# Kernel tuning notes

Hardware: AMD Instinct MI355X
Metric: run time of the kernel (lower is better)

Reference implementation:

```python
import jax, jax.numpy as jnp
import numpy as np

B, TQ, TK, D, H = 4, 2048, 2048, 512, 8  # hidden=512, num_heads=8, head_dim=64


def setup_inputs() -> dict:
    key = jax.random.key(0)
    ks = jax.random.split(key, 7)
    s = 0.03  # small init scale for linear weights
    return {
        "q": jax.random.normal(ks[0], (B, TQ, D), jnp.float32),
        "k": jax.random.normal(ks[1], (B, TK, D), jnp.float32),
        "v": jax.random.normal(ks[2], (B, TK, D), jnp.float32),
        "Wq": jax.random.normal(ks[3], (D, D), jnp.float32) * s,
        "bq": jnp.zeros((D,), jnp.float32),
        "Wk": jax.random.normal(ks[4], (D, D), jnp.float32) * s,
        "bk": jnp.zeros((D,), jnp.float32),
        "Wv": jax.random.normal(ks[5], (D, D), jnp.float32) * s,
        "bv": jnp.zeros((D,), jnp.float32),
        "Wo": jax.random.normal(ks[6], (D, D), jnp.float32) * s,
        "bo": jnp.zeros((D,), jnp.float32),
    }


def reference(q, k, v, Wq, bq, Wk, bk, Wv, bv, Wo, bo):
    Bq, Tq, _ = q.shape
    Tk = k.shape[1]
    Dh = D // H  # head dim = 64
    # torch Linear: x @ W.T + b; split heads -> [B, H, T, Dh]
    qh = (q @ Wq.T + bq).reshape(Bq, Tq, H, Dh).transpose(0, 2, 1, 3)
    kh = (k @ Wk.T + bk).reshape(Bq, Tk, H, Dh).transpose(0, 2, 1, 3)
    vh = (v @ Wv.T + bv).reshape(Bq, Tk, H, Dh).transpose(0, 2, 1, 3)
    scale = 1.0 / float(np.sqrt(Dh))
    scores = jnp.einsum("bhqd,bhkd->bhqk", qh, kh) * scale  # [B,H,Tq,Tk]
    # causal mask: tril(ones, diagonal=Tk-Tq); log-additive masking == -inf off-band
    causal = jnp.tril(jnp.ones((Tq, Tk), bool), k=Tk - Tq)
    scores = jnp.where(causal, scores, -jnp.inf)
    w = jax.nn.softmax(scores, axis=-1)  # attention weights
    x = jnp.einsum("bhqk,bhkd->bhqd", w, vh)
    x = x.transpose(0, 2, 1, 3).reshape(Bq, Tq, D)
    return x @ Wo.T + bo, w
```

## Files before the change

kernel.cpp:

```cpp
#include <hip/hip_runtime.h>


typedef __attribute__((ext_vector_type(4))) float f32x4;
typedef __attribute__((ext_vector_type(8))) short short8;
typedef __attribute__((ext_vector_type(8))) __bf16 bf16x8;
typedef __attribute__((ext_vector_type(2))) unsigned int uintx2;
typedef __attribute__((ext_vector_type(4))) unsigned int uintx4;

static __device__ __forceinline__ unsigned short bfc(float f) {
  return __builtin_bit_cast(unsigned short, (__bf16)f);
}
static __device__ __forceinline__ unsigned pkbf(float a, float b) {
  return (unsigned)bfc(a) | ((unsigned)bfc(b) << 16);
}
static __device__ __forceinline__ short8 cvt_bf8(f32x4 f0, f32x4 f1) {
  uintx4 u;
  u[0] = pkbf(f0[0], f0[1]);
  u[1] = pkbf(f0[2], f0[3]);
  u[2] = pkbf(f1[0], f1[1]);
  u[3] = pkbf(f1[2], f1[3]);
  return __builtin_bit_cast(short8, u);
}

static __device__ __forceinline__ f32x4 mfma16(short8 a, short8 b, f32x4 c) {
  return __builtin_amdgcn_mfma_f32_16x16x32_bf16(
      __builtin_bit_cast(bf16x8, a), __builtin_bit_cast(bf16x8, b), c, 0, 0, 0);
}

#define GLD16(gsrc, ldst)                                                     \
  __builtin_amdgcn_global_load_lds(                                           \
      (const __attribute__((address_space(1))) void*)(gsrc),                  \
      (__attribute__((address_space(3))) void*)(ldst), 16, 0, 0)

template <int IN_BF16>
__device__ __forceinline__ void gemm_core(const void* __restrict__ Xv,
                                          const float* __restrict__ W,
                                          short (*As)[72], short (*Bs)[72],
                                          int row0, int col0, f32x4 (&acc)[4][4]) {
  const int tid = threadIdx.x;
  const int lane = tid & 63;
  const int wv = tid >> 6, wm = wv >> 1, wn = wv & 1;
  const int g = lane >> 4, c = lane & 15;

  for (int k0 = 0; k0 < 512; k0 += 64) {
    for (int ch = tid; ch < 1024; ch += 256) {
      const int r = ch >> 3, kc = (ch & 7) * 8;
      if (IN_BF16) {
        *(short8*)&As[r][kc] =
            *(const short8*)((const short*)Xv + (size_t)(row0 + r) * 512 + k0 + kc);
      } else {
        const float* src = (const float*)Xv + (size_t)(row0 + r) * 512 + k0 + kc;
        *(short8*)&As[r][kc] = cvt_bf8(*(const f32x4*)src, *(const f32x4*)(src + 4));
      }
      {
        const float* src = W + (size_t)(col0 + r) * 512 + k0 + kc;
        *(short8*)&Bs[r][kc] = cvt_bf8(*(const f32x4*)src, *(const f32x4*)(src + 4));
      }
    }
    __syncthreads();
#pragma unroll
    for (int kk = 0; kk < 2; ++kk) {
      short8 a[4], b[4];
#pragma unroll
      for (int i = 0; i < 4; ++i) a[i] = *(const short8*)&As[wm * 64 + i * 16 + c][kk * 32 + g * 8];
#pragma unroll
      for (int i = 0; i < 4; ++i) b[i] = *(const short8*)&Bs[wn * 64 + i * 16 + c][kk * 32 + g * 8];
#pragma unroll
      for (int mi = 0; mi < 4; ++mi)
#pragma unroll
        for (int ni = 0; ni < 4; ++ni) acc[mi][ni] = mfma16(a[mi], b[ni], acc[mi][ni]);
    }
    __syncthreads();
  }
}

__global__ __launch_bounds__(256) void qkv_gemm(
    const float* __restrict__ q, const float* __restrict__ k, const float* __restrict__ v,
    const float* __restrict__ Wq, const float* __restrict__ bq,
    const float* __restrict__ Wk, const float* __restrict__ bk,
    const float* __restrict__ Wv, const float* __restrict__ bv,
    unsigned short* __restrict__ Qbf, unsigned short* __restrict__ Kbf,
    unsigned short* __restrict__ Vbf) {
  __shared__ short As[128][72];
  __shared__ short Bs[128][72];
  const int z = blockIdx.z;
  const float* X = z == 0 ? q : (z == 1 ? k : v);
  const float* W = z == 0 ? Wq : (z == 1 ? Wk : Wv);
  const float* bias = z == 0 ? bq : (z == 1 ? bk : bv);
  const int row0 = blockIdx.x * 128, col0 = blockIdx.y * 128;

  f32x4 acc[4][4] = {};
  gemm_core<0>(X, W, As, Bs, row0, col0, acc);

  const int lane = threadIdx.x & 63;
  const int wv = threadIdx.x >> 6, wm = wv >> 1, wn = wv & 1;
  const int g = lane >> 4, c = lane & 15;

  if (z < 2) {
    unsigned short* Y = z == 0 ? Qbf : Kbf;
    const float scl = z == 0 ? 0.18033688f : 1.0f;
#pragma unroll
    for (int mi = 0; mi < 4; ++mi)
#pragma unroll
      for (int ni = 0; ni < 4; ++ni) {
        const int col = col0 + wn * 64 + ni * 16 + c;
        const float bvl = bias[col];
        const int rowb = row0 + wm * 64 + mi * 16 + g * 4;
#pragma unroll
        for (int r = 0; r < 4; ++r) {
          const int row = rowb + r;
          const int bb = row >> 11, t = row & 2047;
          const int h = col >> 6, dh = col & 63;
          Y[((size_t)((bb * 8 + h) * 2048 + t) << 6) + dh] = bfc((acc[mi][ni][r] + bvl) * scl);
        }
      }
  } else {
#pragma unroll
    for (int mi = 0; mi < 4; ++mi)
#pragma unroll
      for (int ni = 0; ni < 4; ++ni) {
        const int col = col0 + wn * 64 + ni * 16 + c;
        const float bvl = bias[col];
        const int rowb = row0 + wm * 64 + mi * 16 + g * 4;
        const int bb = rowb >> 11, t = rowb & 2047;
        const int h = col >> 6, dh = col & 63;
        uintx2 pk;
        pk[0] = pkbf(acc[mi][ni][0] + bvl, acc[mi][ni][1] + bvl);
        pk[1] = pkbf(acc[mi][ni][2] + bvl, acc[mi][ni][3] + bvl);
        *(uintx2*)(Vbf + ((size_t)((bb * 8 + h) * 64 + dh) * 2048 + t)) = pk;
      }
  }
}

__global__ __launch_bounds__(256) void out_gemm(const unsigned short* __restrict__ ctx,
                                                const float* __restrict__ Wo,
                                                const float* __restrict__ bo,
                                                float* __restrict__ out) {
  __shared__ short As[128][72];
  __shared__ short Bs[128][72];
  const int row0 = blockIdx.x * 128, col0 = blockIdx.y * 128;
  f32x4 acc[4][4] = {};
  gemm_core<1>(ctx, Wo, As, Bs, row0, col0, acc);

  const int lane = threadIdx.x & 63;
  const int wv = threadIdx.x >> 6, wm = wv >> 1, wn = wv & 1;
  const int g = lane >> 4, c = lane & 15;
#pragma unroll
  for (int mi = 0; mi < 4; ++mi)
#pragma unroll
    for (int ni = 0; ni < 4; ++ni) {
      const int col = col0 + wn * 64 + ni * 16 + c;
      const float bvl = bo[col];
      const int rowb = row0 + wm * 64 + mi * 16 + g * 4;
#pragma unroll
      for (int r = 0; r < 4; ++r) out[(size_t)(rowb + r) * 512 + col] = acc[mi][ni][r] + bvl;
    }
}

__global__ __launch_bounds__(256) void attn_kernel(
    const unsigned short* __restrict__ Qb, const unsigned short* __restrict__ Kb,
    const unsigned short* __restrict__ Vtg, unsigned short* __restrict__ ctx,
    float* __restrict__ wout) {
  __shared__ short Kd[2][8192];
  __shared__ short Vd[2][8192];
  __shared__ short Ps[4][16][128];

  const int tid = threadIdx.x, lane = tid & 63, wv = tid >> 6;
  const int g = lane >> 4, c = lane & 15;
  const int sw = (c & 7) << 3;
  const int p = blockIdx.x, bh = blockIdx.y;
  const unsigned short* Qp = Qb + (size_t)bh * (2048 * 64);
  const unsigned short* Kp = Kb + (size_t)bh * (2048 * 64);
  const unsigned short* Vp = Vtg + (size_t)bh * (64 * 2048);
  const int b_ = bh >> 3, h_ = bh & 7;

  for (int half = 0; half < 2; ++half) {
    const int t = half ? (31 - p) : p;
    const int q0 = t * 64;
    const int jmax = t >> 1;
    const int qr = q0 + wv * 16 + c;

    __syncthreads();
#pragma unroll
    for (int i = 0; i < 4; ++i) {
      const int gr = (wv * 4 + i) * 64 + lane;
      const int row = gr >> 3, slot = gr & 7;
      GLD16(Kp + ((size_t)row * 64) + ((slot ^ (row & 7)) << 3),
            (char*)Kd[0] + ((wv * 4 + i) << 10));
    }
#pragma unroll
    for (int i = 0; i < 4; ++i) {
      const int gr = (wv * 4 + i) * 64 + lane;
      const int row = gr >> 4, slot = gr & 15;
      GLD16(Vp + ((size_t)row * 2048) + ((slot ^ (row & 7)) << 3),
            (char*)Vd[0] + ((wv * 4 + i) << 10));
    }

    short8 qf[2];
    qf[0] = *(const short8*)(Qp + (size_t)qr * 64 + g * 8);
    qf[1] = *(const short8*)(Qp + (size_t)qr * 64 + 32 + g * 8);

    f32x4 O[4] = {};
    float l_r = 0.0f;

    for (int j = 0; j <= jmax; ++j) {
      __syncthreads();
      if (j < jmax) {
        const int nb = (j + 1) & 1;
#pragma unroll
        for (int i = 0; i < 4; ++i) {
          const int gr = (wv * 4 + i) * 64 + lane;
          const int row = gr >> 3, slot = gr & 7;
          GLD16(Kp + ((size_t)((j + 1) * 128 + row) * 64) + ((slot ^ (row & 7)) << 3),
                (char*)Kd[nb] + ((wv * 4 + i) << 10));
        }
#pragma unroll
        for (int i = 0; i < 4; ++i) {
          const int gr = (wv * 4 + i) * 64 + lane;
          const int row = gr >> 4, slot = gr & 15;
          GLD16(Vp + ((size_t)row * 2048) + (j + 1) * 128 + ((slot ^ (row & 7)) << 3),
                (char*)Vd[nb] + ((wv * 4 + i) << 10));
        }
      }
      const short* Ksb = Kd[j & 1];
      const short* Vsb = Vd[j & 1];

      f32x4 S[8];
#pragma unroll
      for (int nc = 0; nc < 8; ++nc) S[nc] = (f32x4){0.f, 0.f, 0.f, 0.f};
#pragma unroll
      for (int kk = 0; kk < 2; ++kk)
#pragma unroll
        for (int nc = 0; nc < 8; ++nc) {
          const int row = nc * 16 + c;
          const short8 kf = *(const short8*)&Ksb[row * 64 + (((kk * 4 + g) ^ (c & 7)) << 3)];
          S[nc] = mfma16(kf, qf[kk], S[nc]);
        }

      f32x4 ssum = {0.f, 0.f, 0.f, 0.f};
      if (j == jmax) {
        const int kvb = j * 128 + g * 4;
#pragma unroll
        for (int nc = 0; nc < 8; ++nc) {
#pragma unroll
          for (int r = 0; r < 4; ++r) {
            float val = __builtin_amdgcn_exp2f(S[nc][r]);
            if (kvb + nc * 16 + r > qr) val = 0.f;
            S[nc][r] = val;
          }
          ssum += S[nc];
        }
      } else {
#pragma unroll
        for (int nc = 0; nc < 8; ++nc) {
#pragma unroll
          for (int r = 0; r < 4; ++r) S[nc][r] = __builtin_amdgcn_exp2f(S[nc][r]);
          ssum += S[nc];
        }
      }
      l_r += ssum[0] + ssum[1] + ssum[2] + ssum[3];

#pragma unroll
      for (int nc = 0; nc < 8; ++nc) {
        uintx2 pk;
        pk[0] = pkbf(S[nc][0], S[nc][1]);
        pk[1] = pkbf(S[nc][2], S[nc][3]);
        *(uintx2*)&Ps[wv][c][(nc * 16 + g * 4) ^ sw] = pk;
      }

#pragma unroll
      for (int kk2 = 0; kk2 < 4; ++kk2) {
        const short8 pa = *(const short8*)&Ps[wv][c][(kk2 * 32 + g * 8) ^ sw];
#pragma unroll
        for (int nd = 0; nd < 4; ++nd) {
          const int row = nd * 16 + c;
          const short8 vb = *(const short8*)&Vsb[row * 128 + (((kk2 * 4 + g) ^ (c & 7)) << 3)];
          O[nd] = mfma16(pa, vb, O[nd]);
        }
      }
    }

    l_r += __shfl_xor(l_r, 16);
    l_r += __shfl_xor(l_r, 32);

    {
      float lv[4];
#pragma unroll
      for (int r = 0; r < 4; ++r) lv[r] = __shfl(l_r, g * 4 + r);
#pragma unroll
      for (int r = 0; r < 4; ++r) {
        const float inv = 1.0f / lv[r];
        const int trow = q0 + wv * 16 + g * 4 + r;
        unsigned short* cp = ctx + ((size_t)(b_ * 2048 + trow) * 512) + h_ * 64;
#pragma unroll
        for (int nd = 0; nd < 4; ++nd) cp[nd * 16 + c] = bfc(O[nd][r] * inv);
      }
    }

    const float inv_l = 1.0f / l_r;
    float* wbase = wout + ((size_t)bh * 2048 + q0) * 2048;
    for (int j = jmax; j >= 0; --j) {
      __syncthreads();
      if (j > 0) {
#pragma unroll
        for (int i = 0; i < 4; ++i) {
          const int gr = (wv * 4 + i) * 64 + lane;
          const int row = gr >> 3, slot = gr & 7;
          GLD16(Kp + ((size_t)((j - 1) * 128 + row) * 64) + ((slot ^ (row & 7)) << 3),
                (char*)Kd[(j - 1) & 1] + ((wv * 4 + i) << 10));
        }
      }
      const short* Ksb = Kd[j & 1];

      f32x4 S[8];
#pragma unroll
      for (int nc = 0; nc < 8; ++nc) S[nc] = (f32x4){0.f, 0.f, 0.f, 0.f};
#pragma unroll
      for (int kk = 0; kk < 2; ++kk)
#pragma unroll
        for (int nc = 0; nc < 8; ++nc) {
          const int row = nc * 16 + c;
          const short8 kf = *(const short8*)&Ksb[row * 64 + (((kk * 4 + g) ^ (c & 7)) << 3)];
          S[nc] = mfma16(kf, qf[kk], S[nc]);
        }

      const bool lastj = (j == jmax);
      float* wr = wbase + (size_t)(wv * 16 + c) * 2048 + j * 128;
#pragma unroll
      for (int nc = 0; nc < 8; ++nc) {
        f32x4 w4;
#pragma unroll
        for (int r = 0; r < 4; ++r) {
          float val = __builtin_amdgcn_exp2f(S[nc][r]) * inv_l;
          if (lastj && (j * 128 + nc * 16 + g * 4 + r > qr)) val = 0.f;
          w4[r] = val;
        }
        *(f32x4*)(wr + nc * 16 + g * 4) = w4;
      }
    }

    {
      const int c0 = (jmax + 1) * 128;
      const f32x4 z = {0.f, 0.f, 0.f, 0.f};
      for (int rr = wv; rr < 64; rr += 4) {
        float* rp = wbase + (size_t)rr * 2048;
        for (int x = c0 + lane * 4; x < 2048; x += 256) *(f32x4*)(rp + x) = z;
      }
    }
  }
}

extern "C" void kernel_launch(void* const* d_in, const int* in_sizes, int n_in,
                              void* d_out, int out_size, void* d_ws, size_t ws_size,
                              hipStream_t stream) {
  const float* q  = (const float*)d_in[0];
  const float* k  = (const float*)d_in[1];
  const float* v  = (const float*)d_in[2];
  const float* Wq = (const float*)d_in[3];
  const float* bq = (const float*)d_in[4];
  const float* Wk = (const float*)d_in[5];
  const float* bk = (const float*)d_in[6];
  const float* Wv = (const float*)d_in[7];
  const float* bv = (const float*)d_in[8];
  const float* Wo = (const float*)d_in[9];
  const float* bo = (const float*)d_in[10];

  unsigned short* Qbf = (unsigned short*)d_ws;
  unsigned short* Kbf = Qbf + (size_t)4194304;
  unsigned short* Vbf = Kbf + (size_t)4194304;
  unsigned short* ctx = Vbf + (size_t)4194304;

  float* out  = (float*)d_out;
  float* wout = out + (size_t)4 * 2048 * 512;

  qkv_gemm<<<dim3(64, 4, 3), 256, 0, stream>>>(q, k, v, Wq, bq, Wk, bk, Wv, bv, Qbf, Kbf, Vbf);
  attn_kernel<<<dim3(16, 32), 256, 0, stream>>>(Qbf, Kbf, Vbf, ctx, wout);
  out_gemm<<<dim3(64, 4), 256, 0, stream>>>(ctx, Wo, bo, out);
}
```

Measured before the change: 240.1 us.

## Fuse long tile's weight-output pass with short tile's forward pass sharing K loads

The attention kernel handles a long and a short query tile per block. It now fuses the long tile's second pass (recompute scores, write normalized weights) into the short tile's forward pass, so each K tile staged into LDS feeds both query tiles. The aim is to cut the number of K tile loads and barrier-separated iterations per block. In exchange it keeps both Q fragment sets live and doubles the score accumulators in the fused loop, which raises register pressure.

```diff
diff --git a/kernel.cpp b/kernel.cpp
--- a/kernel.cpp
+++ b/kernel.cpp
@@ -157,6 +157,27 @@
     }
 }
 
+static __device__ __forceinline__ void stage_k(const unsigned short* __restrict__ Kp,
+                                               short* dst, int j, int wv, int lane) {
+#pragma unroll
+  for (int i = 0; i < 4; ++i) {
+    const int gr = (wv * 4 + i) * 64 + lane;
+    const int row = gr >> 3, slot = gr & 7;
+    GLD16(Kp + ((size_t)(j * 128 + row) * 64) + ((slot ^ (row & 7)) << 3),
+          (char*)dst + ((wv * 4 + i) << 10));
+  }
+}
+static __device__ __forceinline__ void stage_v(const unsigned short* __restrict__ Vp,
+                                               short* dst, int j, int wv, int lane) {
+#pragma unroll
+  for (int i = 0; i < 4; ++i) {
+    const int gr = (wv * 4 + i) * 64 + lane;
+    const int row = gr >> 4, slot = gr & 15;
+    GLD16(Vp + ((size_t)row * 2048) + j * 128 + ((slot ^ (row & 7)) << 3),
+          (char*)dst + ((wv * 4 + i) << 10));
+  }
+}
+
 __global__ __launch_bounds__(256) void attn_kernel(
     const unsigned short* __restrict__ Qb, const unsigned short* __restrict__ Kb,
     const unsigned short* __restrict__ Vtg, unsigned short* __restrict__ ctx,
@@ -174,78 +195,159 @@
   const unsigned short* Vp = Vtg + (size_t)bh * (64 * 2048);
   const int b_ = bh >> 3, h_ = bh & 7;
 
-  for (int half = 0; half < 2; ++half) {
-    const int t = half ? (31 - p) : p;
-    const int q0 = t * 64;
-    const int jmax = t >> 1;
-    const int qr = q0 + wv * 16 + c;
-
+  const int tL = 31 - p, tS = p;
+  const int jL = tL >> 1, jS = tS >> 1;
+  const int q0L = tL * 64, q0S = tS * 64;
+  const int qrL = q0L + wv * 16 + c, qrS = q0S + wv * 16 + c;
+
+  short8 qfL[2], qfS[2];
+  qfL[0] = *(const short8*)(Qp + (size_t)qrL * 64 + g * 8);
+  qfL[1] = *(const short8*)(Qp + (size_t)qrL * 64 + 32 + g * 8);
+  qfS[0] = *(const short8*)(Qp + (size_t)qrS * 64 + g * 8);
+  qfS[1] = *(const short8*)(Qp + (size_t)qrS * 64 + 32 + g * 8);
+
+  float* const wbaseL = wout + ((size_t)bh * 2048 + q0L) * 2048;
+  float* const wbaseS = wout + ((size_t)bh * 2048 + q0S) * 2048;
+
+  stage_k(Kp, Kd[0], 0, wv, lane);
+  stage_v(Vp, Vd[0], 0, wv, lane);
+
+  f32x4 OL[4] = {};
+  float lL = 0.0f;
+  for (int j = 0; j <= jL; ++j) {
     __syncthreads();
-#pragma unroll
-    for (int i = 0; i < 4; ++i) {
-      const int gr = (wv * 4 + i) * 64 + lane;
-      const int row = gr >> 3, slot = gr & 7;
-      GLD16(Kp + ((size_t)row * 64) + ((slot ^ (row & 7)) << 3),
-            (char*)Kd[0] + ((wv * 4 + i) << 10));
-    }
-#pragma unroll
-    for (int i = 0; i < 4; ++i) {
-      const int gr = (wv * 4 + i) * 64 + lane;
-      const int row = gr >> 4, slot = gr & 15;
-      GLD16(Vp + ((size_t)row * 2048) + ((slot ^ (row & 7)) << 3),
-            (char*)Vd[0] + ((wv * 4 + i) << 10));
-    }
-
-    short8 qf[2];
-    qf[0] = *(const short8*)(Qp + (size_t)qr * 64 + g * 8);
-    qf[1] = *(const short8*)(Qp + (size_t)qr * 64 + 32 + g * 8);
-
-    f32x4 O[4] = {};
-    float l_r = 0.0f;
-
-    for (int j = 0; j <= jmax; ++j) {
-      __syncthreads();
-      if (j < jmax) {
-        const int nb = (j + 1) & 1;
-#pragma unroll
-        for (int i = 0; i < 4; ++i) {
-          const int gr = (wv * 4 + i) * 64 + lane;
-          const int row = gr >> 3, slot = gr & 7;
-          GLD16(Kp + ((size_t)((j + 1) * 128 + row) * 64) + ((slot ^ (row & 7)) << 3),
-                (char*)Kd[nb] + ((wv * 4 + i) << 10));
-        }
-#pragma unroll
-        for (int i = 0; i < 4; ++i) {
-          const int gr = (wv * 4 + i) * 64 + lane;
-          const int row = gr >> 4, slot = gr & 15;
-          GLD16(Vp + ((size_t)row * 2048) + (j + 1) * 128 + ((slot ^ (row & 7)) << 3),
-                (char*)Vd[nb] + ((wv * 4 + i) << 10));
-        }
-      }
-      const short* Ksb = Kd[j & 1];
+    if (j < jL) {
+      const int nb = (j + 1) & 1;
+      stage_k(Kp, Kd[nb], j + 1, wv, lane);
+      stage_v(Vp, Vd[nb], j + 1, wv, lane);
+    }
+    const short* Ksb = Kd[j & 1];
+    const short* Vsb = Vd[j & 1];
+
+    f32x4 S[8];
+#pragma unroll
+    for (int nc = 0; nc < 8; ++nc) S[nc] = (f32x4){0.f, 0.f, 0.f, 0.f};
+#pragma unroll
+    for (int kk = 0; kk < 2; ++kk)
+#pragma unroll
+      for (int nc = 0; nc < 8; ++nc) {
+        const int row = nc * 16 + c;
+        const short8 kf = *(const short8*)&Ksb[row * 64 + (((kk * 4 + g) ^ (c & 7)) << 3)];
+        S[nc] = mfma16(kf, qfL[kk], S[nc]);
+      }
+
+    f32x4 ssum = {0.f, 0.f, 0.f, 0.f};
+    if (j == jL) {
+      const int kvb = j * 128 + g * 4;
+#pragma unroll
+      for (int nc = 0; nc < 8; ++nc) {
+#pragma unroll
+        for (int r = 0; r < 4; ++r) {
+          float val = __builtin_amdgcn_exp2f(S[nc][r]);
+          if (kvb + nc * 16 + r > qrL) val = 0.f;
+          S[nc][r] = val;
+        }
+        ssum += S[nc];
+      }
+    } else {
+#pragma unroll
+      for (int nc = 0; nc < 8; ++nc) {
+#pragma unroll
+        for (int r = 0; r < 4; ++r) S[nc][r] = __builtin_amdgcn_exp2f(S[nc][r]);
+        ssum += S[nc];
+      }
+    }
+    lL += ssum[0] + ssum[1] + ssum[2] + ssum[3];
+
+#pragma unroll
+    for (int nc = 0; nc < 8; ++nc) {
+      uintx2 pk;
+      pk[0] = pkbf(S[nc][0], S[nc][1]);
+      pk[1] = pkbf(S[nc][2], S[nc][3]);
+      *(uintx2*)&Ps[wv][c][(nc * 16 + g * 4) ^ sw] = pk;
+    }
+#pragma unroll
+    for (int kk2 = 0; kk2 < 4; ++kk2) {
+      const short8 pa = *(const short8*)&Ps[wv][c][(kk2 * 32 + g * 8) ^ sw];
+#pragma unroll
+      for (int nd = 0; nd < 4; ++nd) {
+        const int row = nd * 16 + c;
+        const short8 vb = *(const short8*)&Vsb[row * 128 + (((kk2 * 4 + g) ^ (c & 7)) << 3)];
+        OL[nd] = mfma16(pa, vb, OL[nd]);
+      }
+    }
+  }
+
+  lL += __shfl_xor(lL, 16);
+  lL += __shfl_xor(lL, 32);
+  {
+    float lv[4];
+#pragma unroll
+    for (int r = 0; r < 4; ++r) lv[r] = __shfl(lL, g * 4 + r);
+#pragma unroll
+    for (int r = 0; r < 4; ++r) {
+      const float inv = 1.0f / lv[r];
+      const int trow = q0L + wv * 16 + g * 4 + r;
+      unsigned short* cp = ctx + ((size_t)(b_ * 2048 + trow) * 512) + h_ * 64;
+#pragma unroll
+      for (int nd = 0; nd < 4; ++nd) cp[nd * 16 + c] = bfc(OL[nd][r] * inv);
+    }
+  }
+  const float inv_lL = 1.0f / lL;
+
+  __syncthreads();
+  stage_k(Kp, Kd[0], 0, wv, lane);
+  stage_v(Vp, Vd[0], 0, wv, lane);
+
+  f32x4 OS[4] = {};
+  float lS = 0.0f;
+  for (int j = 0; j <= jL; ++j) {
+    __syncthreads();
+    if (j < jL) {
+      const int nb = (j + 1) & 1;
+      stage_k(Kp, Kd[nb], j + 1, wv, lane);
+      if (j + 1 <= jS) stage_v(Vp, Vd[nb], j + 1, wv, lane);
+    }
+    const short* Ksb = Kd[j & 1];
+
+    if (j <= jS) {
       const short* Vsb = Vd[j & 1];
-
-      f32x4 S[8];
-#pragma unroll
-      for (int nc = 0; nc < 8; ++nc) S[nc] = (f32x4){0.f, 0.f, 0.f, 0.f};
+      f32x4 S[8], S2[8];
+#pragma unroll
+      for (int nc = 0; nc < 8; ++nc) {
+        S[nc] = (f32x4){0.f, 0.f, 0.f, 0.f};
+        S2[nc] = (f32x4){0.f, 0.f, 0.f, 0.f};
+      }
 #pragma unroll
       for (int kk = 0; kk < 2; ++kk)
 #pragma unroll
         for (int nc = 0; nc < 8; ++nc) {
           const int row = nc * 16 + c;
           const short8 kf = *(const short8*)&Ksb[row * 64 + (((kk * 4 + g) ^ (c & 7)) << 3)];
-          S[nc] = mfma16(kf, qf[kk], S[nc]);
-        }
+          S[nc] = mfma16(kf, qfS[kk], S[nc]);
+          S2[nc] = mfma16(kf, qfL[kk], S2[nc]);
+        }
+
+      {
+        float* wr = wbaseL + (size_t)(wv * 16 + c) * 2048 + j * 128;
+#pragma unroll
+        for (int nc = 0; nc < 8; ++nc) {
+          f32x4 w4;
+#pragma unroll
+          for (int r = 0; r < 4; ++r) w4[r] = __builtin_amdgcn_exp2f(S2[nc][r]) * inv_lL;
+          *(f32x4*)(wr + nc * 16 + g * 4) = w4;
+        }
+      }
 
       f32x4 ssum = {0.f, 0.f, 0.f, 0.f};
-      if (j == jmax) {
+      if (j == jS) {
         const int kvb = j * 128 + g * 4;
 #pragma unroll
         for (int nc = 0; nc < 8; ++nc) {
 #pragma unroll
           for (int r = 0; r < 4; ++r) {
             float val = __builtin_amdgcn_exp2f(S[nc][r]);
-            if (kvb + nc * 16 + r > qr) val = 0.f;
+            if (kvb + nc * 16 + r > qrS) val = 0.f;
             S[nc][r] = val;
           }
           ssum += S[nc];
@@ -258,7 +360,7 @@
           ssum += S[nc];
         }
       }
-      l_r += ssum[0] + ssum[1] + ssum[2] + ssum[3];
+      lS += ssum[0] + ssum[1] + ssum[2] + ssum[3];
 
 #pragma unroll
       for (int nc = 0; nc < 8; ++nc) {
@@ -267,7 +369,6 @@
         pk[1] = pkbf(S[nc][2], S[nc][3]);
         *(uintx2*)&Ps[wv][c][(nc * 16 + g * 4) ^ sw] = pk;
       }
-
 #pragma unroll
       for (int kk2 = 0; kk2 < 4; ++kk2) {
         const short8 pa = *(const short8*)&Ps[wv][c][(kk2 * 32 + g * 8) ^ sw];
@@ -275,77 +376,98 @@
         for (int nd = 0; nd < 4; ++nd) {
           const int row = nd * 16 + c;
           const short8 vb = *(const short8*)&Vsb[row * 128 + (((kk2 * 4 + g) ^ (c & 7)) << 3)];
-          O[nd] = mfma16(pa, vb, O[nd]);
-        }
-      }
-    }
-
-    l_r += __shfl_xor(l_r, 16);
-    l_r += __shfl_xor(l_r, 32);
-
-    {
-      float lv[4];
-#pragma unroll
-      for (int r = 0; r < 4; ++r) lv[r] = __shfl(l_r, g * 4 + r);
-#pragma unroll
-      for (int r = 0; r < 4; ++r) {
-        const float inv = 1.0f / lv[r];
-        const int trow = q0 + wv * 16 + g * 4 + r;
-        unsigned short* cp = ctx + ((size_t)(b_ * 2048 + trow) * 512) + h_ * 64;
-#pragma unroll
-        for (int nd = 0; nd < 4; ++nd) cp[nd * 16 + c] = bfc(O[nd][r] * inv);
-      }
-    }
-
-    const float inv_l = 1.0f / l_r;
-    float* wbase = wout + ((size_t)bh * 2048 + q0) * 2048;
-    for (int j = jmax; j >= 0; --j) {
-      __syncthreads();
-      if (j > 0) {
-#pragma unroll
-        for (int i = 0; i < 4; ++i) {
-          const int gr = (wv * 4 + i) * 64 + lane;
-          const int row = gr >> 3, slot = gr & 7;
-          GLD16(Kp + ((size_t)((j - 1) * 128 + row) * 64) + ((slot ^ (row & 7)) << 3),
-                (char*)Kd[(j - 1) & 1] + ((wv * 4 + i) << 10));
-        }
-      }
-      const short* Ksb = Kd[j & 1];
-
-      f32x4 S[8];
-#pragma unroll
-      for (int nc = 0; nc < 8; ++nc) S[nc] = (f32x4){0.f, 0.f, 0.f, 0.f};
+          OS[nd] = mfma16(pa, vb, OS[nd]);
+        }
+      }
+    } else {
+      f32x4 S2[8];
+#pragma unroll
+      for (int nc = 0; nc < 8; ++nc) S2[nc] = (f32x4){0.f, 0.f, 0.f, 0.f};
 #pragma unroll
       for (int kk = 0; kk < 2; ++kk)
 #pragma unroll
         for (int nc = 0; nc < 8; ++nc) {
           const int row = nc * 16 + c;
           const short8 kf = *(const short8*)&Ksb[row * 64 + (((kk * 4 + g) ^ (c & 7)) << 3)];
-          S[nc] = mfma16(kf, qf[kk], S[nc]);
-        }
-
-      const bool lastj = (j == jmax);
-      float* wr = wbase + (size_t)(wv * 16 + c) * 2048 + j * 128;
+          S2[nc] = mfma16(kf, qfL[kk], S2[nc]);
+        }
+      const bool lastj = (j == jL);
+      float* wr = wbaseL + (size_t)(wv * 16 + c) * 2048 + j * 128;
 #pragma unroll
       for (int nc = 0; nc < 8; ++nc) {
         f32x4 w4;
 #pragma unroll
         for (int r = 0; r < 4; ++r) {
-          float val = __builtin_amdgcn_exp2f(S[nc][r]) * inv_l;
-          if (lastj && (j * 128 + nc * 16 + g * 4 + r > qr)) val = 0.f;
+          float val = __builtin_amdgcn_exp2f(S2[nc][r]) * inv_lL;
+          if (lastj && (j * 128 + nc * 16 + g * 4 + r > qrL)) val = 0.f;
           w4[r] = val;
         }
         *(f32x4*)(wr + nc * 16 + g * 4) = w4;
       }
     }
-
-    {
-      const int c0 = (jmax + 1) * 128;
-      const f32x4 z = {0.f, 0.f, 0.f, 0.f};
-      for (int rr = wv; rr < 64; rr += 4) {
-        float* rp = wbase + (size_t)rr * 2048;
-        for (int x = c0 + lane * 4; x < 2048; x += 256) *(f32x4*)(rp + x) = z;
-      }
+  }
+
+  lS += __shfl_xor(lS, 16);
+  lS += __shfl_xor(lS, 32);
+  {
+    float lv[4];
+#pragma unroll
+    for (int r = 0; r < 4; ++r) lv[r] = __shfl(lS, g * 4 + r);
+#pragma unroll
+    for (int r = 0; r < 4; ++r) {
+      const float inv = 1.0f / lv[r];
+      const int trow = q0S + wv * 16 + g * 4 + r;
+      unsigned short* cp = ctx + ((size_t)(b_ * 2048 + trow) * 512) + h_ * 64;
+#pragma unroll
+      for (int nd = 0; nd < 4; ++nd) cp[nd * 16 + c] = bfc(OS[nd][r] * inv);
+    }
+  }
+  const float inv_lS = 1.0f / lS;
+
+  __syncthreads();
+  stage_k(Kp, Kd[0], 0, wv, lane);
+  for (int j = 0; j <= jS; ++j) {
+    __syncthreads();
+    if (j < jS) stage_k(Kp, Kd[(j + 1) & 1], j + 1, wv, lane);
+    const short* Ksb = Kd[j & 1];
+
+    f32x4 S2[8];
+#pragma unroll
+    for (int nc = 0; nc < 8; ++nc) S2[nc] = (f32x4){0.f, 0.f, 0.f, 0.f};
+#pragma unroll
+    for (int kk = 0; kk < 2; ++kk)
+#pragma unroll
+      for (int nc = 0; nc < 8; ++nc) {
+        const int row = nc * 16 + c;
+        const short8 kf = *(const short8*)&Ksb[row * 64 + (((kk * 4 + g) ^ (c & 7)) << 3)];
+        S2[nc] = mfma16(kf, qfS[kk], S2[nc]);
+      }
+    const bool lastj = (j == jS);
+    float* wr = wbaseS + (size_t)(wv * 16 + c) * 2048 + j * 128;
+#pragma unroll
+    for (int nc = 0; nc < 8; ++nc) {
+      f32x4 w4;
+#pragma unroll
+      for (int r = 0; r < 4; ++r) {
+        float val = __builtin_amdgcn_exp2f(S2[nc][r]) * inv_lS;
+        if (lastj && (j * 128 + nc * 16 + g * 4 + r > qrS)) val = 0.f;
+        w4[r] = val;
+      }
+      *(f32x4*)(wr + nc * 16 + g * 4) = w4;
+    }
+  }
+
+  {
+    const f32x4 z = {0.f, 0.f, 0.f, 0.f};
+    const int c0L = (jL + 1) * 128;
+    for (int rr = wv; rr < 64; rr += 4) {
+      float* rp = wbaseL + (size_t)rr * 2048;
+      for (int x = c0L + lane * 4; x < 2048; x += 256) *(f32x4*)(rp + x) = z;
+    }
+    const int c0S = (jS + 1) * 128;
+    for (int rr = wv; rr < 64; rr += 4) {
+      float* rp = wbaseS + (size_t)rr * 2048;
+      for (int x = c0S + lane * 4; x < 2048; x += 256) *(f32x4*)(rp + x) = z;
     }
   }
 }
```

Result: slower. 268.5 us (+11.9%).

## Shrink attention KV tile to 64 columns, raise occupancy, use nontemporal weight stores

Applied to the files above, without the earlier changes.

The attention kernel's key/value tile shrinks from 128 to 64 columns, which halves the LDS buffers, and launch bounds now request 4 blocks per SM for more occupancy. The causal diagonal block now matches the 64-row query tile, so less masked work is computed on the last block. The attention-weight and zero-fill stores become nontemporal to avoid polluting the cache. The cost is twice as many loop iterations and barriers, plus possible register pressure from the occupancy bound.

```diff
diff --git a/kernel.cpp b/kernel.cpp
--- a/kernel.cpp
+++ b/kernel.cpp
@@ -157,13 +157,34 @@
     }
 }
 
-__global__ __launch_bounds__(256) void attn_kernel(
+static __device__ __forceinline__ void stage_k64(const unsigned short* __restrict__ Kp,
+                                                 short* dst, int j, int wv, int lane) {
+#pragma unroll
+  for (int i = 0; i < 2; ++i) {
+    const int gr = (wv * 2 + i) * 64 + lane;
+    const int row = gr >> 3, slot = gr & 7;
+    GLD16(Kp + ((size_t)(j * 64 + row) * 64) + ((slot ^ (row & 7)) << 3),
+          (char*)dst + ((wv * 2 + i) << 10));
+  }
+}
+static __device__ __forceinline__ void stage_v64(const unsigned short* __restrict__ Vp,
+                                                 short* dst, int j, int wv, int lane) {
+#pragma unroll
+  for (int i = 0; i < 2; ++i) {
+    const int gr = (wv * 2 + i) * 64 + lane;
+    const int row = gr >> 3, slot = gr & 7;
+    GLD16(Vp + ((size_t)row * 2048) + j * 64 + ((slot ^ (row & 7)) << 3),
+          (char*)dst + ((wv * 2 + i) << 10));
+  }
+}
+
+__global__ __launch_bounds__(256, 4) void attn_kernel(
     const unsigned short* __restrict__ Qb, const unsigned short* __restrict__ Kb,
     const unsigned short* __restrict__ Vtg, unsigned short* __restrict__ ctx,
     float* __restrict__ wout) {
-  __shared__ short Kd[2][8192];
-  __shared__ short Vd[2][8192];
-  __shared__ short Ps[4][16][128];
+  __shared__ short Kd[2][4096];
+  __shared__ short Vd[2][4096];
+  __shared__ short Ps[4][16][64];
 
   const int tid = threadIdx.x, lane = tid & 63, wv = tid >> 6;
   const int g = lane >> 4, c = lane & 15;
@@ -177,24 +198,12 @@
   for (int half = 0; half < 2; ++half) {
     const int t = half ? (31 - p) : p;
     const int q0 = t * 64;
-    const int jmax = t >> 1;
+    const int jmax = t;
     const int qr = q0 + wv * 16 + c;
 
     __syncthreads();
-#pragma unroll
-    for (int i = 0; i < 4; ++i) {
-      const int gr = (wv * 4 + i) * 64 + lane;
-      const int row = gr >> 3, slot = gr & 7;
-      GLD16(Kp + ((size_t)row * 64) + ((slot ^ (row & 7)) << 3),
-            (char*)Kd[0] + ((wv * 4 + i) << 10));
-    }
-#pragma unroll
-    for (int i = 0; i < 4; ++i) {
-      const int gr = (wv * 4 + i) * 64 + lane;
-      const int row = gr >> 4, slot = gr & 15;
-      GLD16(Vp + ((size_t)row * 2048) + ((slot ^ (row & 7)) << 3),
-            (char*)Vd[0] + ((wv * 4 + i) << 10));
-    }
+    stage_k64(Kp, Kd[0], 0, wv, lane);
+    stage_v64(Vp, Vd[0], 0, wv, lane);
 
     short8 qf[2];
     qf[0] = *(const short8*)(Qp + (size_t)qr * 64 + g * 8);
@@ -207,31 +216,19 @@
       __syncthreads();
       if (j < jmax) {
         const int nb = (j + 1) & 1;
-#pragma unroll
-        for (int i = 0; i < 4; ++i) {
-          const int gr = (wv * 4 + i) * 64 + lane;
-          const int row = gr >> 3, slot = gr & 7;
-          GLD16(Kp + ((size_t)((j + 1) * 128 + row) * 64) + ((slot ^ (row & 7)) << 3),
-                (char*)Kd[nb] + ((wv * 4 + i) << 10));
-        }
-#pragma unroll
-        for (int i = 0; i < 4; ++i) {
-          const int gr = (wv * 4 + i) * 64 + lane;
-          const int row = gr >> 4, slot = gr & 15;
-          GLD16(Vp + ((size_t)row * 2048) + (j + 1) * 128 + ((slot ^ (row & 7)) << 3),
-                (char*)Vd[nb] + ((wv * 4 + i) << 10));
-        }
+        stage_k64(Kp, Kd[nb], j + 1, wv, lane);
+        stage_v64(Vp, Vd[nb], j + 1, wv, lane);
       }
       const short* Ksb = Kd[j & 1];
       const short* Vsb = Vd[j & 1];
 
-      f32x4 S[8];
-#pragma unroll
-      for (int nc = 0; nc < 8; ++nc) S[nc] = (f32x4){0.f, 0.f, 0.f, 0.f};
+      f32x4 S[4];
+#pragma unroll
+      for (int nc = 0; nc < 4; ++nc) S[nc] = (f32x4){0.f, 0.f, 0.f, 0.f};
 #pragma unroll
       for (int kk = 0; kk < 2; ++kk)
 #pragma unroll
-        for (int nc = 0; nc < 8; ++nc) {
+        for (int nc = 0; nc < 4; ++nc) {
           const int row = nc * 16 + c;
           const short8 kf = *(const short8*)&Ksb[row * 64 + (((kk * 4 + g) ^ (c & 7)) << 3)];
           S[nc] = mfma16(kf, qf[kk], S[nc]);
@@ -239,9 +236,9 @@
 
       f32x4 ssum = {0.f, 0.f, 0.f, 0.f};
       if (j == jmax) {
-        const int kvb = j * 128 + g * 4;
-#pragma unroll
-        for (int nc = 0; nc < 8; ++nc) {
+        const int kvb = j * 64 + g * 4;
+#pragma unroll
+        for (int nc = 0; nc < 4; ++nc) {
 #pragma unroll
           for (int r = 0; r < 4; ++r) {
             float val = __builtin_amdgcn_exp2f(S[nc][r]);
@@ -252,7 +249,7 @@
         }
       } else {
 #pragma unroll
-        for (int nc = 0; nc < 8; ++nc) {
+        for (int nc = 0; nc < 4; ++nc) {
 #pragma unroll
           for (int r = 0; r < 4; ++r) S[nc][r] = __builtin_amdgcn_exp2f(S[nc][r]);
           ssum += S[nc];
@@ -261,7 +258,7 @@
       l_r += ssum[0] + ssum[1] + ssum[2] + ssum[3];
 
 #pragma unroll
-      for (int nc = 0; nc < 8; ++nc) {
+      for (int nc = 0; nc < 4; ++nc) {
         uintx2 pk;
         pk[0] = pkbf(S[nc][0], S[nc][1]);
         pk[1] = pkbf(S[nc][2], S[nc][3]);
@@ -269,12 +266,12 @@
       }
 
 #pragma unroll
-      for (int kk2 = 0; kk2 < 4; ++kk2) {
+      for (int kk2 = 0; kk2 < 2; ++kk2) {
         const short8 pa = *(const short8*)&Ps[wv][c][(kk2 * 32 + g * 8) ^ sw];
 #pragma unroll
         for (int nd = 0; nd < 4; ++nd) {
           const int row = nd * 16 + c;
-          const short8 vb = *(const short8*)&Vsb[row * 128 + (((kk2 * 4 + g) ^ (c & 7)) << 3)];
+          const short8 vb = *(const short8*)&Vsb[row * 64 + (((kk2 * 4 + g) ^ (c & 7)) << 3)];
           O[nd] = mfma16(pa, vb, O[nd]);
         }
       }
@@ -301,50 +298,43 @@
     float* wbase = wout + ((size_t)bh * 2048 + q0) * 2048;
     for (int j = jmax; j >= 0; --j) {
       __syncthreads();
-      if (j > 0) {
-#pragma unroll
-        for (int i = 0; i < 4; ++i) {
-          const int gr = (wv * 4 + i) * 64 + lane;
-          const int row = gr >> 3, slot = gr & 7;
-          GLD16(Kp + ((size_t)((j - 1) * 128 + row) * 64) + ((slot ^ (row & 7)) << 3),
-                (char*)Kd[(j - 1) & 1] + ((wv * 4 + i) << 10));
-        }
-      }
+      if (j > 0) stage_k64(Kp, Kd[(j - 1) & 1], j - 1, wv, lane);
       const short* Ksb = Kd[j & 1];
 
-      f32x4 S[8];
-#pragma unroll
-      for (int nc = 0; nc < 8; ++nc) S[nc] = (f32x4){0.f, 0.f, 0.f, 0.f};
+      f32x4 S[4];
+#pragma unroll
+      for (int nc = 0; nc < 4; ++nc) S[nc] = (f32x4){0.f, 0.f, 0.f, 0.f};
 #pragma unroll
       for (int kk = 0; kk < 2; ++kk)
 #pragma unroll
-        for (int nc = 0; nc < 8; ++nc) {
+        for (int nc = 0; nc < 4; ++nc) {
           const int row = nc * 16 + c;
           const short8 kf = *(const short8*)&Ksb[row * 64 + (((kk * 4 + g) ^ (c & 7)) << 3)];
           S[nc] = mfma16(kf, qf[kk], S[nc]);
         }
 
       const bool lastj = (j == jmax);
-      float* wr = wbase + (size_t)(wv * 16 + c) * 2048 + j * 128;
-#pragma unroll
-      for (int nc = 0; nc < 8; ++nc) {
+      float* wr = wbase + (size_t)(wv * 16 + c) * 2048 + j * 64;
+#pragma unroll
+      for (int nc = 0; nc < 4; ++nc) {
         f32x4 w4;
 #pragma unroll
         for (int r = 0; r < 4; ++r) {
           float val = __builtin_amdgcn_exp2f(S[nc][r]) * inv_l;
-          if (lastj && (j * 128 + nc * 16 + g * 4 + r > qr)) val = 0.f;
+          if (lastj && (j * 64 + nc * 16 + g * 4 + r > qr)) val = 0.f;
           w4[r] = val;
         }
-        *(f32x4*)(wr + nc * 16 + g * 4) = w4;
+        __builtin_nontemporal_store(w4, (f32x4*)(wr + nc * 16 + g * 4));
       }
     }
 
     {
-      const int c0 = (jmax + 1) * 128;
+      const int c0 = (jmax + 1) * 64;
       const f32x4 z = {0.f, 0.f, 0.f, 0.f};
       for (int rr = wv; rr < 64; rr += 4) {
         float* rp = wbase + (size_t)rr * 2048;
-        for (int x = c0 + lane * 4; x < 2048; x += 256) *(f32x4*)(rp + x) = z;
+        for (int x = c0 + lane * 4; x < 2048; x += 256)
+          __builtin_nontemporal_store(z, (f32x4*)(rp + x));
       }
     }
   }
```

Result: slower. 245.5 us (+2.3%).
